# Kernel optimization log

Measured on AMD Instinct MI355X. Metric: run time of the kernel, lower is better.

Reference implementation:

```python
import jax, jax.numpy as jnp
import numpy as np

E, H, F, N, B = 512, 8, 2048, 1024, 4
HD = E // H


def setup_inputs() -> dict:
    key = jax.random.key(0)
    ks = jax.random.split(key, 20)
    s = 0.02
    return {
        "node_inputs": jax.random.normal(ks[0], (N, B, E), jnp.float32),
        "parent_mask": jax.random.uniform(ks[1], (B, N, N), jnp.float32),
        "hidden": jax.random.bernoulli(ks[2], 0.5, (B, N, N)),
        "pad_mask": jax.random.bernoulli(ks[3], 0.1, (B, N)),
        "Wp": jax.random.normal(ks[4], (H, E), jnp.float32) * s,
        "bp": jnp.zeros((H,), jnp.float32),
        "Wc": jax.random.normal(ks[5], (H, E), jnp.float32) * s,
        "bc": jnp.zeros((H,), jnp.float32),
        "Wqkv": jax.random.normal(ks[6], (3 * E, E), jnp.float32) * s,
        "bqkv": jnp.zeros((3 * E,), jnp.float32),
        "Wo": jax.random.normal(ks[7], (E, E), jnp.float32) * s,
        "bo": jnp.zeros((E,), jnp.float32),
        "W1": jax.random.normal(ks[8], (F, E), jnp.float32) * s,
        "b1": jnp.zeros((F,), jnp.float32),
        "W2": jax.random.normal(ks[9], (E, F), jnp.float32) * s,
        "b2": jnp.zeros((E,), jnp.float32),
        "ln1_g": jnp.ones((E,), jnp.float32),
        "ln1_b": jnp.zeros((E,), jnp.float32),
        "ln2_g": jnp.ones((E,), jnp.float32),
        "ln2_b": jnp.zeros((E,), jnp.float32),
    }


def _layer_norm(x, g, b, eps=1e-5):
    m = jnp.mean(x, axis=-1, keepdims=True)
    v = jnp.mean((x - m) ** 2, axis=-1, keepdims=True)
    return (x - m) * jax.lax.rsqrt(v + eps) * g + b


def reference(node_inputs, parent_mask, hidden, pad_mask, Wp, bp, Wc, bc,
              Wqkv, bqkv, Wo, bo, W1, b1, W2, b2, ln1_g, ln1_b, ln2_g, ln2_b):
    x = node_inputs  # (N, B, E), seq-first like nn.TransformerEncoderLayer
    # parent/child per-head biases: Linear(E->H), permuted to (B, H, N)
    pbias = jnp.transpose(x @ Wp.T + bp, (1, 2, 0))
    cbias = jnp.transpose(x @ Wc.T + bc, (1, 2, 0))
    # additive attention bias (B, H, N, N)
    am = (jnp.swapaxes(parent_mask, 1, 2)[:, None] * pbias[..., None]
          + parent_mask[:, None] * cbias[..., None])
    am = jnp.where(hidden[:, None], -jnp.inf, am)
    # multi-head self-attention
    qkv = x @ Wqkv.T + bqkv  # (N, B, 3E)
    q, k, v = jnp.split(qkv, 3, axis=-1)

    def heads(t):  # (N, B, E) -> (B, H, N, HD)
        return jnp.transpose(t.reshape(N, B, H, HD), (1, 2, 0, 3))

    q, k, v = heads(q), heads(k), heads(v)
    scores = jnp.einsum("bhqd,bhkd->bhqk", q, k) / jnp.sqrt(jnp.float32(HD)) + am
    scores = jnp.where(pad_mask[:, None, None, :], -jnp.inf, scores)
    attn = jax.nn.softmax(scores, axis=-1)
    ctx = jnp.einsum("bhqk,bhkd->bhqd", attn, v)  # (B, H, N, HD)
    ctx = jnp.transpose(ctx, (2, 0, 1, 3)).reshape(N, B, E)
    attn_out = ctx @ Wo.T + bo
    # post-norm transformer encoder layer (dropout=0, relu activation)
    y = _layer_norm(x + attn_out, ln1_g, ln1_b)
    ff = jax.nn.relu(y @ W1.T + b1) @ W2.T + b2
    return _layer_norm(y + ff, ln2_g, ln2_b)
```

## Files before the change

### kernel.cpp

```cpp
#include <hip/hip_runtime.h>
#include <hip/hip_bf16.h>
#include <stdint.h>

using bf16 = __hip_bfloat16;

typedef __bf16 bf16x8 __attribute__((ext_vector_type(8)));
typedef float  f32x4  __attribute__((ext_vector_type(4)));

__device__ __forceinline__ float bflo(uint32_t u) { return __uint_as_float(u << 16); }
__device__ __forceinline__ float bfhi(uint32_t u) { return __uint_as_float(u & 0xffff0000u); }

__device__ __forceinline__ void load8(const bf16* p, float* f) {
  uint4 u = *(const uint4*)p;
  f[0] = bflo(u.x); f[1] = bfhi(u.x);
  f[2] = bflo(u.y); f[3] = bfhi(u.y);
  f[4] = bflo(u.z); f[5] = bfhi(u.z);
  f[6] = bflo(u.w); f[7] = bfhi(u.w);
}
__device__ __forceinline__ void load8(const float* p, float* f) {
  float4 a = *(const float4*)p, b = *(const float4*)(p + 4);
  f[0] = a.x; f[1] = a.y; f[2] = a.z; f[3] = a.w;
  f[4] = b.x; f[5] = b.y; f[6] = b.z; f[7] = b.w;
}
__device__ __forceinline__ void store1(float* o, float v) { *o = v; }
__device__ __forceinline__ void store1(bf16* o, float v) { *o = __float2bfloat16(v); }
__device__ __forceinline__ uint32_t bfbits(float x) {
  bf16 v = __float2bfloat16(x);
  return (uint32_t)*(uint16_t*)&v;
}

typedef const uint32_t __attribute__((address_space(1)))* gp_t;
typedef uint32_t __attribute__((address_space(3)))* lp_t;
__device__ __forceinline__ void gload16(const void* g, void* l) {
  __builtin_amdgcn_global_load_lds((gp_t)g, (lp_t)l, 16, 0, 0);
}

__global__ __launch_bounds__(256)
void cvt5(const float* __restrict__ s0, const float* __restrict__ s1,
          const float* __restrict__ s2, const float* __restrict__ s3,
          const float* __restrict__ s4, bf16* __restrict__ d0,
          bf16* __restrict__ d1, bf16* __restrict__ d2,
          bf16* __restrict__ d3, bf16* __restrict__ d4)
{
  size_t j = ((size_t)blockIdx.x * 256 + threadIdx.x) * 8;
  const float* s; bf16* o; size_t off;
  if      (j < 2097152) { s = s0; o = d0; off = j; }
  else if (j < 2883584) { s = s1; o = d1; off = j - 2097152; }
  else if (j < 3145728) { s = s2; o = d2; off = j - 2883584; }
  else if (j < 4194304) { s = s3; o = d3; off = j - 3145728; }
  else                  { s = s4; o = d4; off = j - 4194304; }
  float f[8];
  load8(s + off, f);
  uint4 u;
  u.x = (bfbits(f[1]) << 16) | bfbits(f[0]);
  u.y = (bfbits(f[3]) << 16) | bfbits(f[2]);
  u.z = (bfbits(f[5]) << 16) | bfbits(f[4]);
  u.w = (bfbits(f[7]) << 16) | bfbits(f[6]);
  *(uint4*)(o + off) = u;
}

__global__ __launch_bounds__(256)
void mask_pack(const float* __restrict__ pm, const int* __restrict__ hid,
               const int* __restrict__ padm, uint32_t* __restrict__ out)
{
  __shared__ float tileT[128][65];
  const int b = blockIdx.z, q0 = blockIdx.y * 64, k0 = blockIdx.x * 128;
  const int t = threadIdx.x;
  const size_t pb = (size_t)b << 20;
#pragma unroll
  for (int i = 0; i < 32; ++i) {
    int idx = t + i * 256;
    int r = idx >> 6, c = idx & 63;
    tileT[r][c] = pm[pb + (size_t)(k0 + r) * 1024 + q0 + c];
  }
  __syncthreads();
#pragma unroll
  for (int i = 0; i < 32; ++i) {
    int idx = t + i * 256;
    int q = idx >> 7, k = idx & 127;
    size_t src = pb + (size_t)(q0 + q) * 1024 + k0 + k;
    int msk = hid[src] | padm[b * 1024 + k0 + k];
    uint32_t u = 0xFFFFFFFFu;
    if (!msk) u = (bfbits(tileT[k][q]) << 16) | bfbits(pm[src]);
    out[src] = u;
  }
}

template<int MODE, int BN>
__global__ __launch_bounds__(256)
void gemm_bt(const bf16* __restrict__ A, const bf16* __restrict__ W,
             const float* __restrict__ bias, bf16* __restrict__ outb,
             float* __restrict__ outf, int M, int Nout, int K, int kLen)
{
  constexpr int NT = BN / 32;
  __shared__ bf16 As[128 * 64];
  __shared__ bf16 Bs[BN * 64];
  const int t = threadIdx.x, lane = t & 63, wave = t >> 6;
  const int m0 = blockIdx.y * 128, n0 = blockIdx.x * BN;
  const int kOff = blockIdx.z * kLen;
  if (MODE == 3) outf += (size_t)blockIdx.z * M * Nout;
  const int wr = wave >> 1, wc = wave & 1;
  const int frow = lane & 15, ksel = (lane >> 4) * 8;
  f32x4 acc[4 * NT] = {};
  const bf16* Ab = A + (size_t)m0 * K;
  const bf16* Wb = W + (size_t)n0 * K;

  for (int k0 = kOff; k0 < kOff + kLen; k0 += 64) {
    __syncthreads();
#pragma unroll
    for (int i = 0; i < 4; ++i) {
      int ib = i * 256 + wave * 64;
      int idx = ib + lane;
      gload16(Ab + (size_t)(idx >> 3) * K + k0 + (idx & 7) * 8, As + ib * 8);
    }
#pragma unroll
    for (int i = 0; i < BN / 32; ++i) {
      int ib = i * 256 + wave * 64;
      int idx = ib + lane;
      gload16(Wb + (size_t)(idx >> 3) * K + k0 + (idx & 7) * 8, Bs + ib * 8);
    }
    __syncthreads();
#pragma unroll
    for (int kk = 0; kk < 64; kk += 32) {
      bf16x8 af[4], bf_[NT];
#pragma unroll
      for (int mt = 0; mt < 4; ++mt)
        af[mt] = *(const bf16x8*)(As + (wr * 64 + mt * 16 + frow) * 64 + kk + ksel);
#pragma unroll
      for (int nt = 0; nt < NT; ++nt)
        bf_[nt] = *(const bf16x8*)(Bs + (wc * (BN / 2) + nt * 16 + frow) * 64 + kk + ksel);
#pragma unroll
      for (int mt = 0; mt < 4; ++mt)
#pragma unroll
        for (int nt = 0; nt < NT; ++nt)
          acc[mt * NT + nt] = __builtin_amdgcn_mfma_f32_16x16x32_bf16(
              af[mt], bf_[nt], acc[mt * NT + nt], 0, 0, 0);
    }
  }
  const int rb = (lane >> 4) * 4, cb = lane & 15;
#pragma unroll
  for (int mt = 0; mt < 4; ++mt)
#pragma unroll
    for (int nt = 0; nt < NT; ++nt) {
      f32x4 a = acc[mt * NT + nt];
#pragma unroll
      for (int r = 0; r < 4; ++r) {
        int row = m0 + wr * 64 + mt * 16 + rb + r;
        int col = n0 + wc * (BN / 2) + nt * 16 + cb;
        if (MODE == 3) {
          outf[(size_t)row * Nout + col] = a[r];
        } else {
          float v = a[r] + bias[col];
          if (MODE == 1) v = fmaxf(v, 0.f);
          if (MODE == 2) {
            int which = col >> 9, hh = (col >> 6) & 7, d = col & 63;
            int n = row >> 2, b = row & 3;
            size_t idx;
            if (which == 2)
              idx = (((size_t)(64 + b * 8 + hh)) << 16) + (size_t)d * 1024 + n;
            else
              idx = (((size_t)(which * 32 + b * 8 + hh)) << 16) + (size_t)n * 64 + d;
            outb[idx] = __float2bfloat16(v);
          } else {
            outb[(size_t)row * Nout + col] = __float2bfloat16(v);
          }
        }
      }
    }
}

__global__ __launch_bounds__(256)
void pbcb_kernel(const float* __restrict__ x, const float* __restrict__ Wp,
                 const float* __restrict__ bp, const float* __restrict__ Wc,
                 const float* __restrict__ bc, float* __restrict__ pbo,
                 float* __restrict__ cbo)
{
  const int wave = threadIdx.x >> 6, lane = threadIdx.x & 63;
  const int m = blockIdx.x * 4 + wave;
  float xv[8];
  load8(x + (size_t)m * 512 + lane * 8, xv);
  const int n = m >> 2, b = m & 3;
#pragma unroll
  for (int hh = 0; hh < 8; ++hh) {
    float wp[8], wc[8];
    load8(Wp + (size_t)hh * 512 + lane * 8, wp);
    load8(Wc + (size_t)hh * 512 + lane * 8, wc);
    float ap = 0.f, ac = 0.f;
#pragma unroll
    for (int j = 0; j < 8; ++j) { ap += xv[j] * wp[j]; ac += xv[j] * wc[j]; }
#pragma unroll
    for (int off = 32; off; off >>= 1) {
      ap += __shfl_xor(ap, off);
      ac += __shfl_xor(ac, off);
    }
    if (lane == 0) {
      pbo[((size_t)b * 8 + hh) * 1024 + n] = ap + bp[hh];
      cbo[((size_t)b * 8 + hh) * 1024 + n] = ac + bc[hh];
    }
  }
}

__global__ __launch_bounds__(256, 2)
void attn_mfma(const bf16* __restrict__ qkv, const float* __restrict__ pbw,
               const float* __restrict__ cbw, const uint32_t* __restrict__ mpk,
               bf16* __restrict__ ctxo)
{
  __shared__ bf16 Kt[128][80];
  __shared__ bf16 Vt[64][144];
  __shared__ bf16 Ps[4][16][144];
  const int t = threadIdx.x, lane = t & 63, wave = t >> 6;
  const int g = lane >> 4, c = lane & 15;
  const int h = blockIdx.y, b = blockIdx.z;
  const int q0 = blockIdx.x * 64 + wave * 16;
  const size_t bh = (size_t)b * 8 + h;
  const bf16* Qp = qkv + (bh << 16);
  const bf16* Kp = qkv + ((32 + bh) << 16);
  const bf16* Vg = qkv + ((64 + bh) << 16);

  bf16x8 qa0 = *(const bf16x8*)(Qp + (size_t)(q0 + c) * 64 + g * 8);
  bf16x8 qa1 = *(const bf16x8*)(Qp + (size_t)(q0 + c) * 64 + 32 + g * 8);

  const float pbq = pbw[bh * 1024 + q0 + c];
  const float cbq = cbw[bh * 1024 + q0 + c];
  const uint32_t* mrp = mpk + (((size_t)b * 1024 + q0 + c) << 10);

  f32x4 oacc[4] = {{0,0,0,0},{0,0,0,0},{0,0,0,0},{0,0,0,0}};
  float m = -1e30f, l = 0.f;

  for (int kt = 0; kt < 8; ++kt) {
    const int k0 = kt * 128;
    uint4 mu[8];
#pragma unroll
    for (int nt = 0; nt < 8; ++nt)
      mu[nt] = *(const uint4*)(mrp + k0 + nt * 16 + 4 * g);
    __syncthreads();
#pragma unroll
    for (int i = 0; i < 4; ++i) {
      int idx = t + i * 256;
      int r = idx >> 3, cc = idx & 7;
      *(uint4*)&Kt[r][cc * 8] = *(const uint4*)(Kp + (size_t)(k0 + r) * 64 + cc * 8);
    }
#pragma unroll
    for (int i = 0; i < 4; ++i) {
      int idx = t + i * 256;
      int r = idx >> 4, cc = idx & 15;
      *(uint4*)&Vt[r][cc * 8] = *(const uint4*)(Vg + (size_t)r * 1024 + k0 + cc * 8);
    }
    __syncthreads();
    f32x4 sacc[8];
#pragma unroll
    for (int nt = 0; nt < 8; ++nt) {
      f32x4 z = {0.f,0.f,0.f,0.f};
      bf16x8 k0f = *(const bf16x8*)&Kt[nt * 16 + c][g * 8];
      bf16x8 k1f = *(const bf16x8*)&Kt[nt * 16 + c][32 + g * 8];
      z = __builtin_amdgcn_mfma_f32_16x16x32_bf16(k0f, qa0, z, 0, 0, 0);
      z = __builtin_amdgcn_mfma_f32_16x16x32_bf16(k1f, qa1, z, 0, 0, 0);
      sacc[nt] = z;
    }
    float mx = -1e30f;
#pragma unroll
    for (int nt = 0; nt < 8; ++nt) {
      uint32_t uu[4] = {mu[nt].x, mu[nt].y, mu[nt].z, mu[nt].w};
#pragma unroll
      for (int r = 0; r < 4; ++r) {
        float s = sacc[nt][r] * 0.125f + bfhi(uu[r]) * pbq + bflo(uu[r]) * cbq;
        s = (uu[r] == 0xFFFFFFFFu) ? -1e30f : s;
        sacc[nt][r] = s;
        mx = fmaxf(mx, s);
      }
    }
    mx = fmaxf(mx, __shfl_xor(mx, 16));
    mx = fmaxf(mx, __shfl_xor(mx, 32));
    const float newm = fmaxf(m, mx);
    const float al = __expf(m - newm);
    float ps = 0.f;
#pragma unroll
    for (int nt = 0; nt < 8; ++nt) {
      float p0 = (sacc[nt][0] <= -1e29f) ? 0.f : __expf(sacc[nt][0] - newm);
      float p1 = (sacc[nt][1] <= -1e29f) ? 0.f : __expf(sacc[nt][1] - newm);
      float p2 = (sacc[nt][2] <= -1e29f) ? 0.f : __expf(sacc[nt][2] - newm);
      float p3 = (sacc[nt][3] <= -1e29f) ? 0.f : __expf(sacc[nt][3] - newm);
      ps += (p0 + p1) + (p2 + p3);
      uint2 w;
      w.x = (bfbits(p1) << 16) | bfbits(p0);
      w.y = (bfbits(p3) << 16) | bfbits(p2);
      *(uint2*)&Ps[wave][c][nt * 16 + 4 * g] = w;
    }
    ps += __shfl_xor(ps, 16);
    ps += __shfl_xor(ps, 32);
    l = l * al + ps;
    m = newm;
#pragma unroll
    for (int dt = 0; dt < 4; ++dt) {
      oacc[dt][0] *= al; oacc[dt][1] *= al;
      oacc[dt][2] *= al; oacc[dt][3] *= al;
    }
#pragma unroll
    for (int dt = 0; dt < 4; ++dt) {
#pragma unroll
      for (int kc = 0; kc < 4; ++kc) {
        bf16x8 vf = *(const bf16x8*)&Vt[dt * 16 + c][kc * 32 + g * 8];
        bf16x8 pf = *(const bf16x8*)&Ps[wave][c][kc * 32 + g * 8];
        oacc[dt] = __builtin_amdgcn_mfma_f32_16x16x32_bf16(vf, pf, oacc[dt], 0, 0, 0);
      }
    }
  }
  const float inv = (l > 0.f) ? 1.f / l : 0.f;
  const int qg = q0 + c;
#pragma unroll
  for (int dt = 0; dt < 4; ++dt)
#pragma unroll
    for (int rg = 0; rg < 4; ++rg) {
      int d = dt * 16 + 4 * g + rg;
      ctxo[((size_t)qg * 4 + b) * 512 + h * 64 + d] =
          __float2bfloat16(oacc[dt][rg] * inv);
    }
}

template<typename TA, typename TO>
__global__ __launch_bounds__(256)
void ln_res2(const TA* __restrict__ a, const float* __restrict__ p0,
             const float* __restrict__ p1, const float* __restrict__ bias,
             const float* __restrict__ g, const float* __restrict__ be,
             TO* __restrict__ out)
{
  const int wave = threadIdx.x >> 6, lane = threadIdx.x & 63;
  const int m = blockIdx.x * 4 + wave;
  const size_t base = (size_t)m * 512 + lane * 8;
  float va[8], f0[8], f1[8], bb[8];
  load8(a + base, va);
  load8(p0 + base, f0);
  load8(p1 + base, f1);
  load8(bias + lane * 8, bb);
  float v[8], s = 0.f;
#pragma unroll
  for (int j = 0; j < 8; ++j) { v[j] = va[j] + f0[j] + f1[j] + bb[j]; s += v[j]; }
#pragma unroll
  for (int off = 32; off; off >>= 1) s += __shfl_xor(s, off);
  const float mean = s * (1.f / 512.f);
  float q = 0.f;
#pragma unroll
  for (int j = 0; j < 8; ++j) { float d = v[j] - mean; q += d * d; }
#pragma unroll
  for (int off = 32; off; off >>= 1) q += __shfl_xor(q, off);
  const float rs = rsqrtf(q * (1.f / 512.f) + 1e-5f);
  float gv[8], bv[8];
  load8(g + lane * 8, gv);
  load8(be + lane * 8, bv);
#pragma unroll
  for (int j = 0; j < 8; ++j)
    store1(out + base + j, (v[j] - mean) * rs * gv[j] + bv[j]);
}

extern "C" void kernel_launch(void* const* d_in, const int* in_sizes, int n_in,
                              void* d_out, int out_size, void* d_ws, size_t ws_size,
                              hipStream_t stream)
{
  (void)in_sizes; (void)n_in; (void)out_size; (void)ws_size;
  const float* x    = (const float*)d_in[0];
  const float* pm   = (const float*)d_in[1];
  const int*   hid  = (const int*)d_in[2];
  const int*   padm = (const int*)d_in[3];
  const float* Wp   = (const float*)d_in[4];
  const float* bp   = (const float*)d_in[5];
  const float* Wc   = (const float*)d_in[6];
  const float* bc   = (const float*)d_in[7];
  const float* Wqkv = (const float*)d_in[8];
  const float* bqkv = (const float*)d_in[9];
  const float* Wo   = (const float*)d_in[10];
  const float* bo   = (const float*)d_in[11];
  const float* W1   = (const float*)d_in[12];
  const float* b1   = (const float*)d_in[13];
  const float* W2   = (const float*)d_in[14];
  const float* b2   = (const float*)d_in[15];
  const float* g1   = (const float*)d_in[16];
  const float* be1  = (const float*)d_in[17];
  const float* g2   = (const float*)d_in[18];
  const float* be2  = (const float*)d_in[19];

  char* ws = (char*)d_ws;
  bf16*     qkvb  = (bf16*)    (ws);
  float*    pbo   = (float*)   (ws + 12582912);
  float*    cbo   = (float*)   (ws + 12713984);
  uint32_t* mpk   = (uint32_t*)(ws + 12845056);
  bf16*     ctx   = (bf16*)    (ws + 29622272);
  float*    part  = (float*)   (ws);
  bf16*     ff1   = (bf16*)    (ws + 16777216);
  bf16*     y     = (bf16*)    (ws + 33816576);
  bf16*     xb    = (bf16*)    (ws + 38010880);
  bf16*     wqkvb = (bf16*)    (ws + 42205184);
  bf16*     wob   = (bf16*)    (ws + 43778048);
  bf16*     w1b   = (bf16*)    (ws + 44302336);
  bf16*     w2b   = (bf16*)    (ws + 46399488);
  float*    part1 = part + (size_t)4096 * 512;

  cvt5<<<2560, 256, 0, stream>>>(x, Wqkv, Wo, W1, W2, xb, wqkvb, wob, w1b, w2b);
  mask_pack<<<dim3(8, 16, 4), 256, 0, stream>>>(pm, hid, padm, mpk);
  pbcb_kernel<<<1024, 256, 0, stream>>>(x, Wp, bp, Wc, bc, pbo, cbo);
  gemm_bt<2, 128><<<dim3(12, 32), 256, 0, stream>>>(xb, wqkvb, bqkv, qkvb, nullptr, 4096, 1536, 512, 512);
  attn_mfma<<<dim3(16, 8, 4), 256, 0, stream>>>(qkvb, pbo, cbo, mpk, ctx);
  gemm_bt<3, 64><<<dim3(8, 32, 2), 256, 0, stream>>>(ctx, wob, nullptr, nullptr, part, 4096, 512, 512, 256);
  ln_res2<float, bf16><<<1024, 256, 0, stream>>>(x, part, part1, bo, g1, be1, y);
  gemm_bt<1, 128><<<dim3(16, 32), 256, 0, stream>>>(y, w1b, b1, ff1, nullptr, 4096, 2048, 512, 512);
  gemm_bt<3, 64><<<dim3(8, 32, 2), 256, 0, stream>>>(ff1, w2b, nullptr, nullptr, part, 4096, 512, 2048, 1024);
  ln_res2<bf16, float><<<1024, 256, 0, stream>>>(y, part, part1, b2, g2, be2, (float*)d_out);
}
```

Baseline: 278.8 us.

## Fuse parent/child bias projection into QKV GEMM and stream K/V directly into LDS

The separate pbcb kernel is removed. The Wp and Wc rows are appended to the QKV weight matrix, padded to 1664 columns, so the QKV GEMM also writes the per-head parent and child biases in fp32. The 1/sqrt(HD) scale is folded into Q in the GEMM epilogue, which removes one multiply per score in the attention kernel. In attention, K and V tiles are loaded through gload16, apparently global-to-LDS loads, into unpadded LDS buffers, and launch bounds are raised to 3 blocks per SM. The costs are extra padded GEMM columns over uninitialized weight rows and possible LDS bank conflicts from the unpadded row strides.

```diff
diff --git a/kernel.cpp b/kernel.cpp
--- a/kernel.cpp
+++ b/kernel.cpp
@@ -60,6 +60,42 @@
 }
 
 __global__ __launch_bounds__(256)
+void prep_small(const float* __restrict__ Wp, const float* __restrict__ Wc,
+                const float* __restrict__ bqkv, const float* __restrict__ bp,
+                const float* __restrict__ bc, bf16* __restrict__ wq,
+                float* __restrict__ bias_ext)
+{
+  if (blockIdx.x < 2) {
+    int j = (blockIdx.x * 256 + threadIdx.x) * 8;
+    if (j < 4096) {
+      float f[8]; load8(Wp + j, f);
+#pragma unroll
+      for (int i = 0; i < 8; ++i) wq[(size_t)1536 * 512 + j + i] = __float2bfloat16(f[i]);
+    }
+  } else if (blockIdx.x < 4) {
+    int j = ((blockIdx.x - 2) * 256 + threadIdx.x) * 8;
+    if (j < 4096) {
+      float f[8]; load8(Wc + j, f);
+#pragma unroll
+      for (int i = 0; i < 8; ++i) wq[(size_t)1544 * 512 + j + i] = __float2bfloat16(f[i]);
+    }
+  } else {
+    int j = threadIdx.x * 8;
+#pragma unroll
+    for (int i = 0; i < 8; ++i) {
+      int cc = j + i;
+      if (cc < 1664) {
+        float v = 0.f;
+        if (cc < 1536) v = bqkv[cc];
+        else if (cc < 1544) v = bp[cc - 1536];
+        else if (cc < 1552) v = bc[cc - 1544];
+        bias_ext[cc] = v;
+      }
+    }
+  }
+}
+
+__global__ __launch_bounds__(256)
 void mask_pack(const float* __restrict__ pm, const int* __restrict__ hid,
                const int* __restrict__ padm, uint32_t* __restrict__ out)
 {
@@ -153,14 +189,22 @@
           float v = a[r] + bias[col];
           if (MODE == 1) v = fmaxf(v, 0.f);
           if (MODE == 2) {
-            int which = col >> 9, hh = (col >> 6) & 7, d = col & 63;
+            if (col >= 1552) continue;
             int n = row >> 2, b = row & 3;
-            size_t idx;
-            if (which == 2)
-              idx = (((size_t)(64 + b * 8 + hh)) << 16) + (size_t)d * 1024 + n;
-            else
-              idx = (((size_t)(which * 32 + b * 8 + hh)) << 16) + (size_t)n * 64 + d;
-            outb[idx] = __float2bfloat16(v);
+            if (col >= 1536) {
+              int j = col - 1536;
+              int hh = j & 7;
+              outf[(j < 8 ? 0 : 32768) + (b * 8 + hh) * 1024 + n] = v;
+            } else {
+              int which = col >> 9, hh = (col >> 6) & 7, d = col & 63;
+              if (which == 0) v *= 0.125f;
+              size_t idx;
+              if (which == 2)
+                idx = (((size_t)(64 + b * 8 + hh)) << 16) + (size_t)d * 1024 + n;
+              else
+                idx = (((size_t)(which * 32 + b * 8 + hh)) << 16) + (size_t)n * 64 + d;
+              outb[idx] = __float2bfloat16(v);
+            }
           } else {
             outb[(size_t)row * Nout + col] = __float2bfloat16(v);
           }
@@ -169,44 +213,13 @@
     }
 }
 
-__global__ __launch_bounds__(256)
-void pbcb_kernel(const float* __restrict__ x, const float* __restrict__ Wp,
-                 const float* __restrict__ bp, const float* __restrict__ Wc,
-                 const float* __restrict__ bc, float* __restrict__ pbo,
-                 float* __restrict__ cbo)
-{
-  const int wave = threadIdx.x >> 6, lane = threadIdx.x & 63;
-  const int m = blockIdx.x * 4 + wave;
-  float xv[8];
-  load8(x + (size_t)m * 512 + lane * 8, xv);
-  const int n = m >> 2, b = m & 3;
-#pragma unroll
-  for (int hh = 0; hh < 8; ++hh) {
-    float wp[8], wc[8];
-    load8(Wp + (size_t)hh * 512 + lane * 8, wp);
-    load8(Wc + (size_t)hh * 512 + lane * 8, wc);
-    float ap = 0.f, ac = 0.f;
-#pragma unroll
-    for (int j = 0; j < 8; ++j) { ap += xv[j] * wp[j]; ac += xv[j] * wc[j]; }
-#pragma unroll
-    for (int off = 32; off; off >>= 1) {
-      ap += __shfl_xor(ap, off);
-      ac += __shfl_xor(ac, off);
-    }
-    if (lane == 0) {
-      pbo[((size_t)b * 8 + hh) * 1024 + n] = ap + bp[hh];
-      cbo[((size_t)b * 8 + hh) * 1024 + n] = ac + bc[hh];
-    }
-  }
-}
-
-__global__ __launch_bounds__(256, 2)
+__global__ __launch_bounds__(256, 3)
 void attn_mfma(const bf16* __restrict__ qkv, const float* __restrict__ pbw,
                const float* __restrict__ cbw, const uint32_t* __restrict__ mpk,
                bf16* __restrict__ ctxo)
 {
-  __shared__ bf16 Kt[128][80];
-  __shared__ bf16 Vt[64][144];
+  __shared__ bf16 Kt[128 * 64];
+  __shared__ bf16 Vt[64 * 128];
   __shared__ bf16 Ps[4][16][144];
   const int t = threadIdx.x, lane = t & 63, wave = t >> 6;
   const int g = lane >> 4, c = lane & 15;
@@ -229,30 +242,30 @@
 
   for (int kt = 0; kt < 8; ++kt) {
     const int k0 = kt * 128;
+    __syncthreads();
+#pragma unroll
+    for (int i = 0; i < 4; ++i) {
+      int ib = i * 256 + wave * 64;
+      int idx = ib + lane;
+      gload16(Kp + (size_t)(k0 + (idx >> 3)) * 64 + (idx & 7) * 8, Kt + ib * 8);
+    }
+#pragma unroll
+    for (int i = 0; i < 4; ++i) {
+      int ib = i * 256 + wave * 64;
+      int idx = ib + lane;
+      gload16(Vg + (size_t)(idx >> 4) * 1024 + k0 + (idx & 15) * 8, Vt + ib * 8);
+    }
     uint4 mu[8];
 #pragma unroll
     for (int nt = 0; nt < 8; ++nt)
       mu[nt] = *(const uint4*)(mrp + k0 + nt * 16 + 4 * g);
     __syncthreads();
-#pragma unroll
-    for (int i = 0; i < 4; ++i) {
-      int idx = t + i * 256;
-      int r = idx >> 3, cc = idx & 7;
-      *(uint4*)&Kt[r][cc * 8] = *(const uint4*)(Kp + (size_t)(k0 + r) * 64 + cc * 8);
-    }
-#pragma unroll
-    for (int i = 0; i < 4; ++i) {
-      int idx = t + i * 256;
-      int r = idx >> 4, cc = idx & 15;
-      *(uint4*)&Vt[r][cc * 8] = *(const uint4*)(Vg + (size_t)r * 1024 + k0 + cc * 8);
-    }
-    __syncthreads();
     f32x4 sacc[8];
 #pragma unroll
     for (int nt = 0; nt < 8; ++nt) {
       f32x4 z = {0.f,0.f,0.f,0.f};
-      bf16x8 k0f = *(const bf16x8*)&Kt[nt * 16 + c][g * 8];
-      bf16x8 k1f = *(const bf16x8*)&Kt[nt * 16 + c][32 + g * 8];
+      bf16x8 k0f = *(const bf16x8*)(Kt + (nt * 16 + c) * 64 + g * 8);
+      bf16x8 k1f = *(const bf16x8*)(Kt + (nt * 16 + c) * 64 + 32 + g * 8);
       z = __builtin_amdgcn_mfma_f32_16x16x32_bf16(k0f, qa0, z, 0, 0, 0);
       z = __builtin_amdgcn_mfma_f32_16x16x32_bf16(k1f, qa1, z, 0, 0, 0);
       sacc[nt] = z;
@@ -263,7 +276,7 @@
       uint32_t uu[4] = {mu[nt].x, mu[nt].y, mu[nt].z, mu[nt].w};
 #pragma unroll
       for (int r = 0; r < 4; ++r) {
-        float s = sacc[nt][r] * 0.125f + bfhi(uu[r]) * pbq + bflo(uu[r]) * cbq;
+        float s = sacc[nt][r] + bfhi(uu[r]) * pbq + bflo(uu[r]) * cbq;
         s = (uu[r] == 0xFFFFFFFFu) ? -1e30f : s;
         sacc[nt][r] = s;
         mx = fmaxf(mx, s);
@@ -299,7 +312,7 @@
     for (int dt = 0; dt < 4; ++dt) {
 #pragma unroll
       for (int kc = 0; kc < 4; ++kc) {
-        bf16x8 vf = *(const bf16x8*)&Vt[dt * 16 + c][kc * 32 + g * 8];
+        bf16x8 vf = *(const bf16x8*)(Vt + (dt * 16 + c) * 128 + kc * 32 + g * 8);
         bf16x8 pf = *(const bf16x8*)&Ps[wave][c][kc * 32 + g * 8];
         oacc[dt] = __builtin_amdgcn_mfma_f32_16x16x32_bf16(vf, pf, oacc[dt], 0, 0, 0);
       }
@@ -389,15 +402,16 @@
   bf16*     y     = (bf16*)    (ws + 33816576);
   bf16*     xb    = (bf16*)    (ws + 38010880);
   bf16*     wqkvb = (bf16*)    (ws + 42205184);
-  bf16*     wob   = (bf16*)    (ws + 43778048);
-  bf16*     w1b   = (bf16*)    (ws + 44302336);
-  bf16*     w2b   = (bf16*)    (ws + 46399488);
+  bf16*     wob   = (bf16*)    (ws + 43909120);
+  bf16*     w1b   = (bf16*)    (ws + 44433408);
+  bf16*     w2b   = (bf16*)    (ws + 46530560);
+  float*    bext  = (float*)   (ws + 48627712);
   float*    part1 = part + (size_t)4096 * 512;
 
   cvt5<<<2560, 256, 0, stream>>>(x, Wqkv, Wo, W1, W2, xb, wqkvb, wob, w1b, w2b);
+  prep_small<<<5, 256, 0, stream>>>(Wp, Wc, bqkv, bp, bc, wqkvb, bext);
   mask_pack<<<dim3(8, 16, 4), 256, 0, stream>>>(pm, hid, padm, mpk);
-  pbcb_kernel<<<1024, 256, 0, stream>>>(x, Wp, bp, Wc, bc, pbo, cbo);
-  gemm_bt<2, 128><<<dim3(12, 32), 256, 0, stream>>>(xb, wqkvb, bqkv, qkvb, nullptr, 4096, 1536, 512, 512);
+  gemm_bt<2, 128><<<dim3(13, 32), 256, 0, stream>>>(xb, wqkvb, bext, qkvb, pbo, 4096, 1664, 512, 512);
   attn_mfma<<<dim3(16, 8, 4), 256, 0, stream>>>(qkvb, pbo, cbo, mpk, ctx);
   gemm_bt<3, 64><<<dim3(8, 32, 2), 256, 0, stream>>>(ctx, wob, nullptr, nullptr, part, 4096, 512, 512, 256);
   ln_res2<float, bf16><<<1024, 256, 0, stream>>>(x, part, part1, bo, g1, be1, y);
```

New measurement: 291.0 us. 1.04x slower.
